# Kernel tuning notes

Hardware: AMD Instinct MI355X
Metric: run time of the kernel (lower is better)

## Reference

```python
import jax, jax.numpy as jnp
import numpy as np

D = 1024          # model_dim
BD = D // 2       # bottleneck_dim
K = 64            # num_splats
B, S = 8, 2048


def setup_inputs() -> dict:
    key = jax.random.key(0)
    ks = jax.random.split(key, 12)
    sc = 0.02
    return {
        "token_embeddings": jax.random.normal(ks[0], (B, S, D), jnp.float32),
        "splat_influences": jax.random.uniform(ks[1], (B, S, K), jnp.float32),
        # encoder: Linear(D -> BD), stored [in, out]
        "enc_W": jax.random.normal(ks[2], (D, BD), jnp.float32) * sc,
        "enc_b": jnp.zeros((BD,), jnp.float32),
        # per-splat transforms: K x Linear(BD -> BD)
        "trans_W": jax.random.normal(ks[3], (K, BD, BD), jnp.float32) * sc,
        "trans_b": jnp.zeros((K, BD), jnp.float32),
        # decoder: Linear(BD -> D)
        "dec_W": jax.random.normal(ks[4], (BD, D), jnp.float32) * sc,
        "dec_b": jnp.zeros((D,), jnp.float32),
        # flow gate: Linear(D -> D) + sigmoid
        "gate_W": jax.random.normal(ks[5], (D, D), jnp.float32) * sc,
        "gate_b": jnp.zeros((D,), jnp.float32),
    }


def reference(token_embeddings, splat_influences, enc_W, enc_b,
              trans_W, trans_b, dec_W, dec_b, gate_W, gate_b):
    # gather: [B,K,S] @ [B,S,D] -> [B,K,D]
    influences_t = jnp.swapaxes(splat_influences, 1, 2)          # [B,K,S]
    gathered = jnp.einsum('bks,bsd->bkd', influences_t, token_embeddings)
    total = jnp.clip(influences_t.sum(axis=2, keepdims=True), 1e-8, None)  # [B,K,1]
    gathered = gathered / total
    # encoder (dropout inactive at eval)
    encoded = jax.nn.relu(gathered @ enc_W + enc_b)              # [B,K,BD]
    # per-splat transform as grouped matmul
    transformed = jnp.einsum('bkd,kde->bke', encoded, trans_W) + trans_b  # [B,K,BD]
    decoded = transformed @ dec_W + dec_b                        # [B,K,D]
    # scatter back to tokens: [B,S,K] @ [B,K,D]
    flow = jnp.einsum('bsk,bkd->bsd', splat_influences, decoded)
    gate = jax.nn.sigmoid(token_embeddings @ gate_W + gate_b)    # [B,S,D]
    return flow * gate
```

## Files before the change

kernel.cpp:

```cpp
#include <hip/hip_runtime.h>

#define BB 8
#define SS 2048
#define DD 1024
#define BDD 512
#define NSP 64

typedef __attribute__((ext_vector_type(8))) short bf16x8;
typedef __attribute__((ext_vector_type(4))) float f32x4;
typedef unsigned short u16;
typedef unsigned int u32;

__device__ __forceinline__ u16 f2bf(float f) {
  u32 u = __builtin_bit_cast(u32, f);
  u = u + 0x7fffu + ((u >> 16) & 1u);
  return (u16)(u >> 16);
}

__device__ __forceinline__ void gl_lds16(const void* g, void* l) {
  __builtin_amdgcn_global_load_lds((const __attribute__((address_space(1))) void*)g,
                                   (__attribute__((address_space(3))) void*)l,
                                   16, 0, 0);
}

__global__ void k_prep(const float* __restrict__ tok, const float* __restrict__ infl,
                       const float* __restrict__ gw, u16* __restrict__ tokbf,
                       u16* __restrict__ tokT, u16* __restrict__ inflbf,
                       u16* __restrict__ inflT, float* __restrict__ rsum,
                       u16* __restrict__ gwt) {
  __shared__ __align__(16) char smraw[64 * 80 * 2 + 32 * 64 * 4];
  u16(*tile)[80] = (u16(*)[80])smraw;
  float(*ps)[64] = (float(*)[64])(smraw + 64 * 80 * 2);
  float(*gt)[33] = (float(*)[33])smraw;
  int bid = blockIdx.x;
  int t = threadIdx.x;

  if (bid < 4096) {
    int C0 = (bid & 15) * 64;
    int R0 = (bid >> 4) * 64;
    int b = R0 >> 11, s0 = R0 & 2047;
    int lr = t >> 3, lc = (t & 7) * 8;
#pragma unroll
    for (int i = 0; i < 2; ++i) {
      int r = lr + i * 32;
      const float* src = tok + (size_t)(R0 + r) * DD + C0 + lc;
      float4 a = *(const float4*)src;
      float4 bq = *(const float4*)(src + 4);
      uint4 v;
      v.x = f2bf(a.x) | ((u32)f2bf(a.y) << 16);
      v.y = f2bf(a.z) | ((u32)f2bf(a.w) << 16);
      v.z = f2bf(bq.x) | ((u32)f2bf(bq.y) << 16);
      v.w = f2bf(bq.z) | ((u32)f2bf(bq.w) << 16);
      *(uint4*)(tokbf + (size_t)(R0 + r) * DD + C0 + lc) = v;
      *(uint4*)&tile[r][lc] = v;
    }
    __syncthreads();
    int sseg = (t & 7) * 8;
#pragma unroll
    for (int i = 0; i < 2; ++i) {
      int dcol = (t >> 3) + i * 32;
      u16 a0 = tile[sseg + 0][dcol], a1 = tile[sseg + 1][dcol];
      u16 a2 = tile[sseg + 2][dcol], a3 = tile[sseg + 3][dcol];
      u16 a4 = tile[sseg + 4][dcol], a5 = tile[sseg + 5][dcol];
      u16 a6 = tile[sseg + 6][dcol], a7 = tile[sseg + 7][dcol];
      uint4 v;
      v.x = a0 | ((u32)a1 << 16);
      v.y = a2 | ((u32)a3 << 16);
      v.z = a4 | ((u32)a5 << 16);
      v.w = a6 | ((u32)a7 << 16);
      *(uint4*)(tokT + (size_t)b * DD * SS + (size_t)(C0 + dcol) * SS + s0 + sseg) = v;
    }
  } else if (bid < 4352) {
    int R0 = (bid - 4096) * 64;
    int b = R0 >> 11, s0 = R0 & 2047;
    int st = s0 >> 6;
    int lr = t >> 3, lc = (t & 7) * 8;
    float col[8];
#pragma unroll
    for (int j = 0; j < 8; ++j) col[j] = 0.f;
#pragma unroll
    for (int i = 0; i < 2; ++i) {
      int r = lr + i * 32;
      const float* src = infl + (size_t)(R0 + r) * NSP + lc;
      float4 a = *(const float4*)src;
      float4 bq = *(const float4*)(src + 4);
      col[0] += a.x; col[1] += a.y; col[2] += a.z; col[3] += a.w;
      col[4] += bq.x; col[5] += bq.y; col[6] += bq.z; col[7] += bq.w;
      uint4 v;
      v.x = f2bf(a.x) | ((u32)f2bf(a.y) << 16);
      v.y = f2bf(a.z) | ((u32)f2bf(a.w) << 16);
      v.z = f2bf(bq.x) | ((u32)f2bf(bq.y) << 16);
      v.w = f2bf(bq.z) | ((u32)f2bf(bq.w) << 16);
      *(uint4*)(inflbf + (size_t)(R0 + r) * NSP + lc) = v;
      *(uint4*)&tile[r][lc] = v;
    }
#pragma unroll
    for (int j = 0; j < 8; ++j) ps[lr][lc + j] = col[j];
    __syncthreads();
    if (t < 64) {
      float s = 0.f;
#pragma unroll
      for (int rr = 0; rr < 32; ++rr) s += ps[rr][t];
      rsum[((size_t)b * 32 + st) * 64 + t] = s;
    }
    int sseg = (t & 7) * 8;
#pragma unroll
    for (int i = 0; i < 2; ++i) {
      int dcol = (t >> 3) + i * 32;
      u16 a0 = tile[sseg + 0][dcol], a1 = tile[sseg + 1][dcol];
      u16 a2 = tile[sseg + 2][dcol], a3 = tile[sseg + 3][dcol];
      u16 a4 = tile[sseg + 4][dcol], a5 = tile[sseg + 5][dcol];
      u16 a6 = tile[sseg + 6][dcol], a7 = tile[sseg + 7][dcol];
      uint4 v;
      v.x = a0 | ((u32)a1 << 16);
      v.y = a2 | ((u32)a3 << 16);
      v.z = a4 | ((u32)a5 << 16);
      v.w = a6 | ((u32)a7 << 16);
      *(uint4*)(inflT + ((size_t)b * NSP + dcol) * SS + s0 + sseg) = v;
    }
  } else {
    int g = bid - 4352;
    int n0 = (g & 31) * 32, k0 = (g >> 5) * 32;
    int tx = t & 31, ty = t >> 5;
#pragma unroll
    for (int r = 0; r < 4; ++r) {
      int kr = ty + r * 8;
      gt[kr][tx] = gw[(k0 + kr) * DD + n0 + tx];
    }
    __syncthreads();
#pragma unroll
    for (int r = 0; r < 4; ++r) {
      int nc = ty + r * 8;
      gwt[(n0 + nc) * DD + k0 + tx] = f2bf(gt[tx][nc]);
    }
  }
}

__global__ __launch_bounds__(256) void k_gather_mfma(const u16* __restrict__ inflT,
                                                     const u16* __restrict__ tokT,
                                                     float* __restrict__ pg) {
  __shared__ u16 As[64 * 64];
  __shared__ u16 Bs[64 * 64];
  int t = threadIdx.x;
  int l = t & 63, w = t >> 6;
  int wr = w >> 1, wc = w & 1;
  int n0 = blockIdx.x * 64;
  int b = blockIdx.y;
  int sq = blockIdx.z;
  int l15 = l & 15, lh = l >> 4;
  int srow = t >> 3, scol = (t & 7) * 8;

  const u16* ap = inflT + (size_t)b * NSP * SS;
  const u16* bp = tokT + (size_t)b * DD * SS;

  f32x4 acc[2][2];
#pragma unroll
  for (int i = 0; i < 2; ++i)
#pragma unroll
    for (int j = 0; j < 2; ++j) acc[i][j] = (f32x4){0.f, 0.f, 0.f, 0.f};

  for (int kt = 0; kt < 8; ++kt) {
    int k0 = sq * 512 + kt * 64;
#pragma unroll
    for (int i = 0; i < 2; ++i) {
      int row = srow + i * 32;
      gl_lds16(ap + row * SS + k0 + scol, &As[row * 64 + scol]);
      gl_lds16(bp + (n0 + row) * SS + k0 + scol, &Bs[row * 64 + scol]);
    }
    __syncthreads();
#pragma unroll
    for (int ks = 0; ks < 2; ++ks) {
      bf16x8 af[2], bfv[2];
#pragma unroll
      for (int mi = 0; mi < 2; ++mi)
        af[mi] = *(const bf16x8*)&As[(wr * 32 + mi * 16 + l15) * 64 + ks * 32 + lh * 8];
#pragma unroll
      for (int ni = 0; ni < 2; ++ni)
        bfv[ni] = *(const bf16x8*)&Bs[(wc * 32 + ni * 16 + l15) * 64 + ks * 32 + lh * 8];
#pragma unroll
      for (int mi = 0; mi < 2; ++mi)
#pragma unroll
        for (int ni = 0; ni < 2; ++ni)
          acc[mi][ni] = __builtin_amdgcn_mfma_f32_16x16x32_bf16(af[mi], bfv[ni], acc[mi][ni], 0, 0, 0);
    }
    __syncthreads();
  }

#pragma unroll
  for (int mi = 0; mi < 2; ++mi)
#pragma unroll
    for (int ni = 0; ni < 2; ++ni)
#pragma unroll
      for (int r = 0; r < 4; ++r) {
        int krow = wr * 32 + mi * 16 + lh * 4 + r;
        int dcol = n0 + wc * 32 + ni * 16 + l15;
        pg[((size_t)sq * 512 + b * NSP + krow) * DD + dcol] = acc[mi][ni][r];
      }
}

__global__ void k_enc_part(const float* __restrict__ pg, const float* __restrict__ rsum,
                           const float* __restrict__ encW, float* __restrict__ pe) {
  __shared__ float gl[8][64];
  int dq = blockIdx.x, mt = blockIdx.y;
  int m0 = mt * 8, d0 = dq * 64;
  int t = threadIdx.x;
  {
    int r = t >> 5, c = t & 31;
    float s1 = 0.f, s2 = 0.f;
#pragma unroll
    for (int q = 0; q < 4; ++q) {
      const float* qp = pg + ((size_t)q * 512 + m0 + r) * DD + d0;
      s1 += qp[c]; s2 += qp[c + 32];
    }
    int mrow = m0 + r;
    int bq = mrow >> 6, kq = mrow & 63;
    float tt = 0.f;
#pragma unroll
    for (int st = 0; st < 32; ++st) tt += rsum[((size_t)bq * 32 + st) * 64 + kq];
    float rt = 1.f / fmaxf(tt, 1e-8f);
    gl[r][c] = s1 * rt;
    gl[r][c + 32] = s2 * rt;
  }
  __syncthreads();
  int n4 = (t & 127) * 4, mh = (t >> 7) * 4;
  float4 acc[4];
#pragma unroll
  for (int m = 0; m < 4; ++m) acc[m] = (float4){0.f, 0.f, 0.f, 0.f};
  for (int i = 0; i < 64; ++i) {
    float4 wv = *(const float4*)(encW + (d0 + i) * BDD + n4);
#pragma unroll
    for (int m = 0; m < 4; ++m) {
      float g = gl[mh + m][i];
      acc[m].x += g * wv.x; acc[m].y += g * wv.y;
      acc[m].z += g * wv.z; acc[m].w += g * wv.w;
    }
  }
#pragma unroll
  for (int m = 0; m < 4; ++m)
    *(float4*)(pe + ((size_t)dq * 512 + m0 + mh + m) * BDD + n4) = acc[m];
}

__global__ void k_trans_part(const float* __restrict__ pe, const float* __restrict__ encB,
                             const float* __restrict__ trW, float* __restrict__ pt) {
  __shared__ float el[8][32];
  int dq = blockIdx.x, ks = blockIdx.y;
  int d0 = dq * 32;
  int t = threadIdx.x;
  {
    int r = t >> 5, c = t & 31;
    int m = r * NSP + ks;
    float s = 0.f;
#pragma unroll
    for (int p = 0; p < 16; ++p)
      s += pe[((size_t)p * 512 + m) * BDD + d0 + c];
    el[r][c] = fmaxf(s + encB[d0 + c], 0.f);
  }
  __syncthreads();
  int n4 = (t & 127) * 4, mh = (t >> 7) * 4;
  float4 acc[4];
#pragma unroll
  for (int m = 0; m < 4; ++m) acc[m] = (float4){0.f, 0.f, 0.f, 0.f};
  for (int i = 0; i < 32; ++i) {
    float4 wv = *(const float4*)(trW + ((size_t)ks * BDD + d0 + i) * BDD + n4);
#pragma unroll
    for (int m = 0; m < 4; ++m) {
      float g = el[mh + m][i];
      acc[m].x += g * wv.x; acc[m].y += g * wv.y;
      acc[m].z += g * wv.z; acc[m].w += g * wv.w;
    }
  }
#pragma unroll
  for (int m = 0; m < 4; ++m)
    *(float4*)(pt + ((size_t)dq * 512 + (mh + m) * NSP + ks) * BDD + n4) = acc[m];
}

__global__ void k_dec_part(const float* __restrict__ pt, const float* __restrict__ trB,
                           const float* __restrict__ decW, float* __restrict__ pd) {
  __shared__ float tl[8][64];
  int dq = blockIdx.x, mt = blockIdx.y;
  int m0 = mt * 8, d0 = dq * 64;
  int t = threadIdx.x;
  {
    int r = t >> 5, c = t & 31;
    int m = m0 + r;
    float s1 = 0.f, s2 = 0.f;
#pragma unroll
    for (int p = 0; p < 16; ++p) {
      const float* qp = pt + ((size_t)p * 512 + m) * BDD + d0;
      s1 += qp[c]; s2 += qp[c + 32];
    }
    tl[r][c] = s1 + trB[(m & 63) * BDD + d0 + c];
    tl[r][c + 32] = s2 + trB[(m & 63) * BDD + d0 + c + 32];
  }
  __syncthreads();
  int n4 = t * 4;
  float4 acc[8];
#pragma unroll
  for (int m = 0; m < 8; ++m) acc[m] = (float4){0.f, 0.f, 0.f, 0.f};
  for (int i = 0; i < 64; ++i) {
    float4 wv = *(const float4*)(decW + (d0 + i) * DD + n4);
#pragma unroll
    for (int m = 0; m < 8; ++m) {
      float g = tl[m][i];
      acc[m].x += g * wv.x; acc[m].y += g * wv.y;
      acc[m].z += g * wv.z; acc[m].w += g * wv.w;
    }
  }
#pragma unroll
  for (int m = 0; m < 8; ++m)
    *(float4*)(pd + ((size_t)dq * 512 + m0 + m) * DD + n4) = acc[m];
}

__global__ void red_dec(const float* __restrict__ pd, const float* __restrict__ decB,
                        u16* __restrict__ decT) {
  __shared__ u16 st[64][34];
  int nt = blockIdx.x, b = blockIdx.y;
  int n0 = nt * 32;
  int t = threadIdx.x;
  int nn = t & 31, kg = t >> 5;
  float db = decB[n0 + nn];
#pragma unroll
  for (int ki = 0; ki < 8; ++ki) {
    int ks = kg * 8 + ki;
    float s = db;
#pragma unroll
    for (int p = 0; p < 8; ++p)
      s += pd[((size_t)p * 512 + b * NSP + ks) * DD + n0 + nn];
    st[ks][nn] = f2bf(s);
  }
  __syncthreads();
  int nr = t >> 3, kseg = (t & 7) * 8;
  uint4 v;
  v.x = st[kseg + 0][nr] | ((u32)st[kseg + 1][nr] << 16);
  v.y = st[kseg + 2][nr] | ((u32)st[kseg + 3][nr] << 16);
  v.z = st[kseg + 4][nr] | ((u32)st[kseg + 5][nr] << 16);
  v.w = st[kseg + 6][nr] | ((u32)st[kseg + 7][nr] << 16);
  *(uint4*)(decT + ((size_t)b * DD + n0 + nr) * NSP + kseg) = v;
}

#define VM2 asm volatile("s_waitcnt vmcnt(2)" ::: "memory");
#define VM0 asm volatile("s_waitcnt vmcnt(0)" ::: "memory");

#define STA(sl, k0, p)                                                        \
  { int e = (p)*512 + t; int row = e >> 3; int cs = ((e & 7) ^ (row & 7)) * 8; \
    gl_lds16(tokbf + (size_t)(m0 + row) * DD + (k0) + cs, &As[sl][e * 8]); }
#define STB(sl, k0, p)                                                        \
  { int e = (p)*512 + t; int row = e >> 3; int cs = ((e & 7) ^ (row & 7)) * 8; \
    gl_lds16(gwt + (size_t)(n0 + row) * DD + (k0) + cs, &Bs[sl][e * 8]); }

#define PH0(sl, CC, ACC, W, STG)                                              \
  {                                                                           \
    W __builtin_amdgcn_s_barrier();                                           \
    bf16x8 af[4];                                                             \
    _Pragma("unroll")                                                         \
    for (int mi_ = 0; mi_ < 4; ++mi_)                                         \
      af[mi_] = *(const bf16x8*)&As[sl][aB + mi_ * 1024 + (CC)];              \
    _Pragma("unroll")                                                         \
    for (int ni_ = 0; ni_ < 4; ++ni_)                                         \
      bfv[ni_] = *(const bf16x8*)&Bs[sl][bB + ni_ * 1024 + (CC)];             \
    STG                                                                       \
    __builtin_amdgcn_s_setprio(1);                                            \
    _Pragma("unroll")                                                         \
    for (int mi_ = 0; mi_ < 4; ++mi_)                                         \
      _Pragma("unroll")                                                       \
      for (int ni_ = 0; ni_ < 4; ++ni_)                                       \
        ACC[mi_][ni_] = __builtin_amdgcn_mfma_f32_16x16x32_bf16(af[mi_], bfv[ni_], ACC[mi_][ni_], 0, 0, 0); \
    __builtin_amdgcn_s_setprio(0);                                            \
  }

#define PH1(sl, CC, ACC, W, STG)                                              \
  {                                                                           \
    W __builtin_amdgcn_s_barrier();                                           \
    bf16x8 af[4];                                                             \
    _Pragma("unroll")                                                         \
    for (int mi_ = 0; mi_ < 4; ++mi_)                                         \
      af[mi_] = *(const bf16x8*)&As[sl][aB + 4096 + mi_ * 1024 + (CC)];       \
    STG                                                                       \
    __builtin_amdgcn_s_setprio(1);                                            \
    _Pragma("unroll")                                                         \
    for (int mi_ = 0; mi_ < 4; ++mi_)                                         \
      _Pragma("unroll")                                                       \
      for (int ni_ = 0; ni_ < 4; ++ni_)                                       \
        ACC[4 + mi_][ni_] = __builtin_amdgcn_mfma_f32_16x16x32_bf16(af[mi_], bfv[ni_], ACC[4 + mi_][ni_], 0, 0, 0); \
    __builtin_amdgcn_s_setprio(0);                                            \
  }

#define GTILE(sl, ACC, W0, W1, S0, S1, S2, S3)                                \
  {                                                                           \
    bf16x8 bfv[4];                                                            \
    PH0(sl, c0, ACC, W0, S0)                                                  \
    PH1(sl, c0, ACC, W1, S1)                                                  \
    PH0(sl, c1, ACC, , S2)                                                    \
    PH1(sl, c1, ACC, , S3)                                                    \
  }

__global__ __launch_bounds__(512, 2) void k_gate(const u16* __restrict__ tokbf,
                                                 const u16* __restrict__ gwt,
                                                 u16* __restrict__ zbf) {
  __shared__ u16 As[2][256 * 64];
  __shared__ u16 Bs[2][256 * 64];
  int t = threadIdx.x;
  int l = t & 63, w = t >> 6;
  int wr = w >> 2, wc = w & 3;
  int bid = blockIdx.x;
  int wg = (bid & 7) * 32 + (bid >> 3);
  int mt = wg & 63, nt = wg >> 6;
  int m0 = mt * 256, n0 = nt * 256;
  int l15 = l & 15, lh = l >> 4;
  int x7 = l15 & 7;
  int c0 = (lh ^ x7) * 8;
  int c1 = ((4 + lh) ^ x7) * 8;
  int aB = (wr * 128 + l15) * 64;
  int bB = (wc * 64 + l15) * 64;

  f32x4 accg[8][4];
#pragma unroll
  for (int i = 0; i < 8; ++i)
#pragma unroll
    for (int j = 0; j < 4; ++j) accg[i][j] = (f32x4){0.f, 0.f, 0.f, 0.f};

  STB(0, 0, 0) STB(0, 0, 1) STB(0, 0, 2) STB(0, 0, 3)
  STA(0, 0, 0) STA(0, 0, 2) STA(0, 0, 1) STA(0, 0, 3)

#pragma unroll 1
  for (int i = 0; i < 7; ++i) {
    int ka = i * 128 + 64;
    int kb = ka + 64;
    GTILE(0, accg, VM2, VM2,
          STB(1, ka, 0) STB(1, ka, 1), STB(1, ka, 2) STB(1, ka, 3),
          STA(1, ka, 0) STA(1, ka, 2), STA(1, ka, 1) STA(1, ka, 3))
    GTILE(1, accg, VM2, VM2,
          STB(0, kb, 0) STB(0, kb, 1), STB(0, kb, 2) STB(0, kb, 3),
          STA(0, kb, 0) STA(0, kb, 2), STA(0, kb, 1) STA(0, kb, 3))
  }
  GTILE(0, accg, VM2, VM2,
        STB(1, 960, 0) STB(1, 960, 1), STB(1, 960, 2) STB(1, 960, 3),
        STA(1, 960, 0) STA(1, 960, 2), STA(1, 960, 1) STA(1, 960, 3))
  GTILE(1, accg, VM2, VM0, , , , )

#pragma unroll
  for (int a = 0; a < 8; ++a)
#pragma unroll
    for (int ni = 0; ni < 4; ++ni)
#pragma unroll
      for (int r = 0; r < 4; ++r) {
        int mr = m0 + wr * 128 + a * 16 + lh * 4 + r;
        int nc = n0 + wc * 64 + ni * 16 + l15;
        zbf[(size_t)mr * DD + nc] = f2bf(accg[a][ni][r]);
      }
}

__global__ __launch_bounds__(256) void k_scat(const u16* __restrict__ inflbf,
                                              const u16* __restrict__ decT,
                                              const u16* __restrict__ zbf,
                                              const float* __restrict__ gateB,
                                              float* __restrict__ outp) {
  __shared__ u16 As[128 * 64];
  __shared__ u16 Bs[128 * 64];
  int t = threadIdx.x;
  int l = t & 63, w = t >> 6;
  int wr = w >> 1, wc = w & 1;
  int m0 = blockIdx.x * 128, n0 = blockIdx.y * 128;
  int l15 = l & 15, lh = l >> 4;
  int b = m0 >> 11, s0m = m0 & 2047;

#pragma unroll
  for (int i = 0; i < 4; ++i) {
    int row = i * 32 + (t >> 3);
    int cs = ((t & 7) ^ (row & 7)) * 8;
    gl_lds16(inflbf + ((size_t)b * SS + s0m + row) * NSP + cs, &As[i * 2048 + t * 8]);
  }
#pragma unroll
  for (int i = 0; i < 4; ++i) {
    int row = i * 32 + (t >> 3);
    int cs = ((t & 7) ^ (row & 7)) * 8;
    gl_lds16(decT + ((size_t)b * DD + n0 + row) * NSP + cs, &Bs[i * 2048 + t * 8]);
  }
  asm volatile("s_waitcnt vmcnt(0)" ::: "memory");
  __builtin_amdgcn_s_barrier();

  f32x4 accf[4][4];
#pragma unroll
  for (int i = 0; i < 4; ++i)
#pragma unroll
    for (int j = 0; j < 4; ++j) accf[i][j] = (f32x4){0.f, 0.f, 0.f, 0.f};
#pragma unroll
  for (int ks = 0; ks < 2; ++ks) {
    bf16x8 af[4], bfv[4];
    int g = ks * 4 + lh;
#pragma unroll
    for (int mi = 0; mi < 4; ++mi) {
      int r = wr * 64 + mi * 16 + l15;
      af[mi] = *(const bf16x8*)&As[r * 64 + (g ^ (r & 7)) * 8];
    }
#pragma unroll
    for (int ni = 0; ni < 4; ++ni) {
      int r = wc * 64 + ni * 16 + l15;
      bfv[ni] = *(const bf16x8*)&Bs[r * 64 + (g ^ (r & 7)) * 8];
    }
#pragma unroll
    for (int mi = 0; mi < 4; ++mi)
#pragma unroll
      for (int ni = 0; ni < 4; ++ni)
        accf[mi][ni] = __builtin_amdgcn_mfma_f32_16x16x32_bf16(af[mi], bfv[ni], accf[mi][ni], 0, 0, 0);
  }

  float gb[4];
#pragma unroll
  for (int ni = 0; ni < 4; ++ni) gb[ni] = gateB[n0 + wc * 64 + ni * 16 + l15];
#pragma unroll
  for (int mi = 0; mi < 4; ++mi)
#pragma unroll
    for (int ni = 0; ni < 4; ++ni)
#pragma unroll
      for (int r = 0; r < 4; ++r) {
        int mr = m0 + wr * 64 + mi * 16 + lh * 4 + r;
        int nc = n0 + wc * 64 + ni * 16 + l15;
        u16 zr = zbf[(size_t)mr * DD + nc];
        float z = __builtin_bit_cast(float, (u32)zr << 16) + gb[ni];
        float gate = 1.f / (1.f + __expf(-z));
        outp[(size_t)mr * DD + nc] = accf[mi][ni][r] * gate;
      }
}

extern "C" void kernel_launch(void* const* d_in, const int* in_sizes, int n_in,
                              void* d_out, int out_size, void* d_ws, size_t ws_size,
                              hipStream_t stream) {
  const float* tok = (const float*)d_in[0];
  const float* infl = (const float*)d_in[1];
  const float* encW = (const float*)d_in[2];
  const float* encB = (const float*)d_in[3];
  const float* trW = (const float*)d_in[4];
  const float* trB = (const float*)d_in[5];
  const float* decW = (const float*)d_in[6];
  const float* decB = (const float*)d_in[7];
  const float* gw = (const float*)d_in[8];
  const float* gateB = (const float*)d_in[9];
  float* outp = (float*)d_out;

  char* wsp = (char*)d_ws;
  u16* tokbf = (u16*)(wsp);
  u16* gwt = (u16*)(wsp + 33554432);
  u16* inflbf = (u16*)(wsp + 35651584);
  u16* decT = (u16*)(wsp + 41945088);
  u16* tokT = (u16*)(wsp + 42993664);
  float* pe = (float*)(wsp + 42993664);
  float* pt = (float*)(wsp + 42993664 + 16777216);
  u16* zbf = (u16*)(wsp + 42993664);
  u16* inflT = (u16*)(wsp + 76548096);
  float* rsum = (float*)(wsp + 78645248);
  float* scratch = (float*)(wsp + 78710784);

  k_prep<<<dim3(5376), dim3(256), 0, stream>>>(tok, infl, gw, tokbf, tokT, inflbf,
                                               inflT, rsum, gwt);
  k_gather_mfma<<<dim3(16, 8, 4), dim3(256), 0, stream>>>(inflT, tokT, scratch);
  k_enc_part<<<dim3(16, 64), dim3(256), 0, stream>>>(scratch, rsum, encW, pe);
  k_trans_part<<<dim3(16, 64), dim3(256), 0, stream>>>(pe, encB, trW, pt);
  k_dec_part<<<dim3(8, 64), dim3(256), 0, stream>>>(pt, trB, decW, scratch);
  red_dec<<<dim3(32, 8), dim3(256), 0, stream>>>(scratch, decB, decT);
  k_gate<<<dim3(256), dim3(512), 0, stream>>>(tokbf, gwt, zbf);
  k_scat<<<dim3(128, 8), dim3(256), 0, stream>>>(inflbf, decT, zbf, gateB, outp);
}
```

Measured before the change: 175.2 us.

## Restructure gate GEMM warp tiling to full-M per wave with quarter-tile phases

Changes the gate GEMM warp layout from a 2x4 grid (each wave 128x64 of output) to 1x8, where each wave covers all 256 rows and 32 columns. The K-tile is processed in four phases over row quarters, each loading both K halves, and each phase now ends with an extra barrier. The intent is to keep B fragments in registers for the whole tile and spread the async global-to-LDS loads evenly across phases with graduated vmcnt waits. The cost is more A-fragment LDS reads per wave and twice as many barriers per tile.

```diff
diff --git a/kernel.cpp b/kernel.cpp
--- a/kernel.cpp
+++ b/kernel.cpp
@@ -338,60 +338,64 @@
   *(uint4*)(decT + ((size_t)b * DD + n0 + nr) * NSP + kseg) = v;
 }
 
-#define VM2 asm volatile("s_waitcnt vmcnt(2)" ::: "memory");
-#define VM0 asm volatile("s_waitcnt vmcnt(0)" ::: "memory");
-
-#define STA(sl, k0, p)                                                        \
+
+#define GVM(n) asm volatile("s_waitcnt vmcnt(" #n ")" ::: "memory");
+
+#define GSTA(sl, k0, p)                                                        \
   { int e = (p)*512 + t; int row = e >> 3; int cs = ((e & 7) ^ (row & 7)) * 8; \
     gl_lds16(tokbf + (size_t)(m0 + row) * DD + (k0) + cs, &As[sl][e * 8]); }
-#define STB(sl, k0, p)                                                        \
+#define GSTB(sl, k0, p)                                                        \
   { int e = (p)*512 + t; int row = e >> 3; int cs = ((e & 7) ^ (row & 7)) * 8; \
     gl_lds16(gwt + (size_t)(n0 + row) * DD + (k0) + cs, &Bs[sl][e * 8]); }
 
-#define PH0(sl, CC, ACC, W, STG)                                              \
-  {                                                                           \
-    W __builtin_amdgcn_s_barrier();                                           \
-    bf16x8 af[4];                                                             \
-    _Pragma("unroll")                                                         \
-    for (int mi_ = 0; mi_ < 4; ++mi_)                                         \
-      af[mi_] = *(const bf16x8*)&As[sl][aB + mi_ * 1024 + (CC)];              \
-    _Pragma("unroll")                                                         \
-    for (int ni_ = 0; ni_ < 4; ++ni_)                                         \
-      bfv[ni_] = *(const bf16x8*)&Bs[sl][bB + ni_ * 1024 + (CC)];             \
-    STG                                                                       \
-    __builtin_amdgcn_s_setprio(1);                                            \
-    _Pragma("unroll")                                                         \
-    for (int mi_ = 0; mi_ < 4; ++mi_)                                         \
-      _Pragma("unroll")                                                       \
-      for (int ni_ = 0; ni_ < 4; ++ni_)                                       \
-        ACC[mi_][ni_] = __builtin_amdgcn_mfma_f32_16x16x32_bf16(af[mi_], bfv[ni_], ACC[mi_][ni_], 0, 0, 0); \
-    __builtin_amdgcn_s_setprio(0);                                            \
-  }
-
-#define PH1(sl, CC, ACC, W, STG)                                              \
-  {                                                                           \
-    W __builtin_amdgcn_s_barrier();                                           \
-    bf16x8 af[4];                                                             \
-    _Pragma("unroll")                                                         \
-    for (int mi_ = 0; mi_ < 4; ++mi_)                                         \
-      af[mi_] = *(const bf16x8*)&As[sl][aB + 4096 + mi_ * 1024 + (CC)];       \
-    STG                                                                       \
-    __builtin_amdgcn_s_setprio(1);                                            \
-    _Pragma("unroll")                                                         \
-    for (int mi_ = 0; mi_ < 4; ++mi_)                                         \
-      _Pragma("unroll")                                                       \
-      for (int ni_ = 0; ni_ < 4; ++ni_)                                       \
-        ACC[4 + mi_][ni_] = __builtin_amdgcn_mfma_f32_16x16x32_bf16(af[mi_], bfv[ni_], ACC[4 + mi_][ni_], 0, 0, 0); \
-    __builtin_amdgcn_s_setprio(0);                                            \
-  }
-
-#define GTILE(sl, ACC, W0, W1, S0, S1, S2, S3)                                \
-  {                                                                           \
-    bf16x8 bfv[4];                                                            \
-    PH0(sl, c0, ACC, W0, S0)                                                  \
-    PH1(sl, c0, ACC, W1, S1)                                                  \
-    PH0(sl, c1, ACC, , S2)                                                    \
-    PH1(sl, c1, ACC, , S3)                                                    \
+#define GLOADB(sl)                                                             \
+  _Pragma("unroll")                                                            \
+  for (int nf = 0; nf < 2; ++nf) {                                             \
+    int br = wc * 32 + nf * 16 + l15;                                          \
+    bfv[nf][0] = *(const bf16x8*)&Bs[sl][br * 64 + c0];                        \
+    bfv[nf][1] = *(const bf16x8*)&Bs[sl][br * 64 + c1];                        \
+  }
+
+#define GPH(sl, mq, VMW, STG, LDB)                                             \
+  {                                                                            \
+    VMW                                                                        \
+    __builtin_amdgcn_s_barrier();                                              \
+    LDB                                                                        \
+    bf16x8 af[4][2];                                                           \
+    _Pragma("unroll")                                                          \
+    for (int mf = 0; mf < 4; ++mf) {                                           \
+      int ar = (mq)*64 + mf * 16 + l15;                                        \
+      af[mf][0] = *(const bf16x8*)&As[sl][ar * 64 + c0];                       \
+      af[mf][1] = *(const bf16x8*)&As[sl][ar * 64 + c1];                       \
+    }                                                                          \
+    STG                                                                        \
+    __builtin_amdgcn_s_setprio(1);                                             \
+    _Pragma("unroll")                                                          \
+    for (int mf = 0; mf < 4; ++mf)                                             \
+      _Pragma("unroll")                                                        \
+      for (int nf = 0; nf < 2; ++nf) {                                         \
+        acc[(mq)*4 + mf][nf] = __builtin_amdgcn_mfma_f32_16x16x32_bf16(af[mf][0], bfv[nf][0], acc[(mq)*4 + mf][nf], 0, 0, 0); \
+        acc[(mq)*4 + mf][nf] = __builtin_amdgcn_mfma_f32_16x16x32_bf16(af[mf][1], bfv[nf][1], acc[(mq)*4 + mf][nf], 0, 0, 0); \
+      }                                                                        \
+    __builtin_amdgcn_s_setprio(0);                                             \
+    __builtin_amdgcn_s_barrier();                                              \
+  }
+
+#define GT_FULL(sl, osl, k1)                                                   \
+  {                                                                            \
+    bf16x8 bfv[2][2];                                                          \
+    GPH(sl, 0, GVM(3), GSTB(osl, k1, 0) GSTB(osl, k1, 1), GLOADB(sl))          \
+    GPH(sl, 1, GVM(4), GSTB(osl, k1, 2) GSTB(osl, k1, 3), )                    \
+    GPH(sl, 2, GVM(5), GSTA(osl, k1, 0) GSTA(osl, k1, 1), )                    \
+    GPH(sl, 3, GVM(6), GSTA(osl, k1, 2) GSTA(osl, k1, 3), )                    \
+  }
+#define GT_LAST(sl)                                                            \
+  {                                                                            \
+    bf16x8 bfv[2][2];                                                          \
+    GPH(sl, 0, GVM(3), , GLOADB(sl))                                           \
+    GPH(sl, 1, GVM(2), , )                                                     \
+    GPH(sl, 2, GVM(1), , )                                                     \
+    GPH(sl, 3, GVM(0), , )                                                     \
   }
 
 __global__ __launch_bounds__(512, 2) void k_gate(const u16* __restrict__ tokbf,
@@ -400,8 +404,7 @@
   __shared__ u16 As[2][256 * 64];
   __shared__ u16 Bs[2][256 * 64];
   int t = threadIdx.x;
-  int l = t & 63, w = t >> 6;
-  int wr = w >> 2, wc = w & 3;
+  int l = t & 63, wc = t >> 6;
   int bid = blockIdx.x;
   int wg = (bid & 7) * 32 + (bid >> 3);
   int mt = wg & 63, nt = wg >> 6;
@@ -410,43 +413,33 @@
   int x7 = l15 & 7;
   int c0 = (lh ^ x7) * 8;
   int c1 = ((4 + lh) ^ x7) * 8;
-  int aB = (wr * 128 + l15) * 64;
-  int bB = (wc * 64 + l15) * 64;
-
-  f32x4 accg[8][4];
-#pragma unroll
-  for (int i = 0; i < 8; ++i)
-#pragma unroll
-    for (int j = 0; j < 4; ++j) accg[i][j] = (f32x4){0.f, 0.f, 0.f, 0.f};
-
-  STB(0, 0, 0) STB(0, 0, 1) STB(0, 0, 2) STB(0, 0, 3)
-  STA(0, 0, 0) STA(0, 0, 2) STA(0, 0, 1) STA(0, 0, 3)
+
+  f32x4 acc[16][2];
+#pragma unroll
+  for (int i = 0; i < 16; ++i)
+#pragma unroll
+    for (int j = 0; j < 2; ++j) acc[i][j] = (f32x4){0.f, 0.f, 0.f, 0.f};
+
+  GSTB(0, 0, 0) GSTB(0, 0, 1) GSTB(0, 0, 2) GSTB(0, 0, 3)
+  GSTA(0, 0, 0) GSTA(0, 0, 1) GSTA(0, 0, 2) GSTA(0, 0, 3)
 
 #pragma unroll 1
   for (int i = 0; i < 7; ++i) {
-    int ka = i * 128 + 64;
-    int kb = ka + 64;
-    GTILE(0, accg, VM2, VM2,
-          STB(1, ka, 0) STB(1, ka, 1), STB(1, ka, 2) STB(1, ka, 3),
-          STA(1, ka, 0) STA(1, ka, 2), STA(1, ka, 1) STA(1, ka, 3))
-    GTILE(1, accg, VM2, VM2,
-          STB(0, kb, 0) STB(0, kb, 1), STB(0, kb, 2) STB(0, kb, 3),
-          STA(0, kb, 0) STA(0, kb, 2), STA(0, kb, 1) STA(0, kb, 3))
-  }
-  GTILE(0, accg, VM2, VM2,
-        STB(1, 960, 0) STB(1, 960, 1), STB(1, 960, 2) STB(1, 960, 3),
-        STA(1, 960, 0) STA(1, 960, 2), STA(1, 960, 1) STA(1, 960, 3))
-  GTILE(1, accg, VM2, VM0, , , , )
-
-#pragma unroll
-  for (int a = 0; a < 8; ++a)
-#pragma unroll
-    for (int ni = 0; ni < 4; ++ni)
+    GT_FULL(0, 1, (2 * i + 1) * 64)
+    GT_FULL(1, 0, (2 * i + 2) * 64)
+  }
+  GT_FULL(0, 1, 960)
+  GT_LAST(1)
+
+#pragma unroll
+  for (int a = 0; a < 16; ++a)
+#pragma unroll
+    for (int nf = 0; nf < 2; ++nf)
 #pragma unroll
       for (int r = 0; r < 4; ++r) {
-        int mr = m0 + wr * 128 + a * 16 + lh * 4 + r;
-        int nc = n0 + wc * 64 + ni * 16 + l15;
-        zbf[(size_t)mr * DD + nc] = f2bf(accg[a][ni][r]);
+        int mr = m0 + a * 16 + lh * 4 + r;
+        int nc = n0 + wc * 32 + nf * 16 + l15;
+        zbf[(size_t)mr * DD + nc] = f2bf(acc[a][nf][r]);
       }
 }
 
```

After: 172.2 us. Within noise of the previous version (-1.7%).
